# Kernel tuning notes

Measured on AMD Instinct MI355X. Metric: run time of the kernel, lower is better.

The kernel has to match this reference:

```python
import jax, jax.numpy as jnp
from jax import lax
import numpy as np

THRESHOLD = 0.9
KHALF = 5  # conv_kernel_size; full conv width = 2*KHALF + 1 = 11


def _cif_scan(eouts, alpha_norm, elens, ylens, Lp1):
    """Vectorized-over-batch integrate-and-fire scan over time (lax.scan)."""
    B, T, D = eouts.shape
    bidx = jnp.arange(B)
    dt = eouts.dtype

    def step(carry, xs):
        alpha_accum, state, n_tok, fired = carry
        a_t, e_t, t = xs  # a_t: [B], e_t: [B,D], t: scalar int
        alpha_accum = alpha_accum + a_t
        active = (t <= elens - 1) & (n_tok < ylens)
        fire = active & (alpha_accum >= THRESHOLD)
        ak1 = 1.0 - alpha_accum
        ak2 = a_t - ak1
        # attention-weight column for time t
        aw_col = jnp.zeros((B, Lp1), dt)
        w_old = jnp.where(fire, ak1, jnp.where(active, a_t, jnp.zeros((), dt)))
        aw_col = aw_col.at[bidx, n_tok].add(w_old)
        n_new = n_tok + fire.astype(n_tok.dtype)
        aw_col = aw_col.at[bidx, n_new].add(jnp.where(fire, ak2, jnp.zeros((), dt)))
        # fired output row (set once per token slot)
        fire_val = state + ak1[:, None] * e_t
        cur = fired[bidx, n_tok]
        fired = fired.at[bidx, n_tok].set(jnp.where(fire[:, None], fire_val, cur))
        # integrate / reset state
        state = jnp.where(fire[:, None], ak2[:, None] * e_t,
                          jnp.where(active[:, None], state + a_t[:, None] * e_t, state))
        alpha_accum = jnp.where(fire, ak2, alpha_accum)
        return (alpha_accum, state, n_new, fired), aw_col

    init = (jnp.zeros((B,), dt), jnp.zeros((B, D), dt),
            jnp.zeros((B,), jnp.int32), jnp.zeros((B, Lp1, D), dt))
    xs = (jnp.swapaxes(alpha_norm, 0, 1), jnp.swapaxes(eouts, 0, 1),
          jnp.arange(T))
    (_, _, _, fired), aw_cols = lax.scan(step, init, xs)
    aws = jnp.transpose(aw_cols, (1, 2, 0))[:, None]  # [B,1,Lp1,T]
    return fired, aws


def _forward(eouts, conv_w, conv_b, proj_w, proj_b, elens, ylens, L):
    # Conv1d over time, 'same' padding: [B,T,D] -> [B,T,C]
    conv_feat = lax.conv_general_dilated(
        eouts, conv_w, window_strides=(1,), padding=[(KHALF, KHALF)],
        dimension_numbers=('NWC', 'WIO', 'NWC')) + conv_b
    alpha = jax.nn.sigmoid(conv_feat @ proj_w + proj_b)[:, :, 0]  # [B,T]
    alpha_norm = alpha / jnp.sum(alpha, axis=1, keepdims=True) \
        * ylens[:, None].astype(alpha.dtype)
    fired, aws = _cif_scan(eouts, alpha_norm, elens, ylens, L + 1)
    return fired[:, :L], alpha, aws


def setup_inputs():
    key = jax.random.key(0)
    k1, k2, k3, k4, k5 = jax.random.split(key, 5)
    B, T, D, C = 16, 2048, 512, 512
    eouts = jax.random.normal(k1, (B, T, D), jnp.float32)
    elens = jnp.maximum(jax.random.randint(k2, (B,), 0, T), T // 2).astype(jnp.int32)
    ylens = jnp.maximum(jax.random.randint(k3, (B,), 0, 128), 32).astype(jnp.int32)
    conv_w = jax.random.normal(k4, (2 * KHALF + 1, D, C), jnp.float32) * 0.02
    conv_b = jnp.zeros((C,), jnp.float32)
    proj_w = jax.random.normal(k5, (C, 1), jnp.float32) * 0.05
    proj_b = jnp.zeros((1,), jnp.float32)
    return dict(eouts=eouts, conv_w=conv_w, conv_b=conv_b,
                proj_w=proj_w, proj_b=proj_b, elens=elens, ylens=ylens)


def reference(eouts, conv_w, conv_b, proj_w, proj_b, elens, ylens):
    L = int(jnp.max(ylens))  # max_len = ylens.max(), as in the original
    return _forward(eouts, conv_w, conv_b, proj_w, proj_b, elens, ylens, L)
```

## Files before the change

kernel.cpp:

```cpp
#include <hip/hip_runtime.h>
#include <math.h>

#define KHALF 5
#define MAXF 256

__global__ void k_prep(const float* __restrict__ conv_w, const float* __restrict__ conv_b,
                       const float* __restrict__ proj_w, const float* __restrict__ proj_b,
                       float* __restrict__ w_eff, float* __restrict__ b_eff,
                       int KD, int C,
                       float* __restrict__ aws, long long awsN, int WB, int NFILL) {
    if ((int)blockIdx.x >= WB) {
        long long N4 = awsN >> 2;
        long long gid = (long long)(blockIdx.x - WB) * 256 + threadIdx.x;
        float4 z = make_float4(0.f, 0.f, 0.f, 0.f);
        float4* a4 = reinterpret_cast<float4*>(aws);
        long long stride = (long long)NFILL * 256;
        for (long long i = gid; i < N4; i += stride) a4[i] = z;
        int tail = (int)(awsN & 3);
        if (gid < tail) aws[4 * N4 + gid] = 0.f;
        return;
    }
    int gid = blockIdx.x * blockDim.x + threadIdx.x;
    int wave = gid >> 6;
    int lane = gid & 63;
    if (wave > KD) return;
    float s = 0.f;
    if (wave < KD) {
        const float* row = conv_w + (size_t)wave * C;
        for (int c = lane * 4; c < C; c += 256) {
            float4 v = *reinterpret_cast<const float4*>(row + c);
            float4 w = *reinterpret_cast<const float4*>(proj_w + c);
            s += v.x * w.x + v.y * w.y + v.z * w.z + v.w * w.w;
        }
    } else {
        for (int c = lane; c < C; c += 64) s += conv_b[c] * proj_w[c];
    }
#pragma unroll
    for (int off = 32; off > 0; off >>= 1) s += __shfl_down(s, off, 64);
    if (lane == 0) {
        if (wave < KD) w_eff[wave] = s;
        else           b_eff[0] = s + proj_b[0];
    }
}

__global__ __launch_bounds__(256) void k_qdot(const float* __restrict__ eouts,
                                              const float* __restrict__ w_eff,
                                              float* __restrict__ q, int BT) {
    __shared__ float tile[64 * 68];
    __shared__ float wls[11 * 68];
    __shared__ float part[64 * 89];
    const int u0 = blockIdx.x * 64;
    const int rp = threadIdx.x & 31;
    const int s8 = threadIdx.x >> 5;
    float acc0[11], acc1[11];
#pragma unroll
    for (int k = 0; k < 11; ++k) { acc0[k] = 0.f; acc1[k] = 0.f; }
    for (int c = 0; c < 8; ++c) {
        __syncthreads();
#pragma unroll
        for (int it = 0; it < 4; ++it) {
            int idx = it * 256 + threadIdx.x;
            int r = idx >> 4, j4 = idx & 15;
            float4 v = *reinterpret_cast<const float4*>(
                eouts + (size_t)(u0 + r) * 512 + c * 64 + j4 * 4);
            *reinterpret_cast<float4*>(&tile[r * 68 + j4 * 4]) = v;
        }
        if (threadIdx.x < 176) {
            int k = threadIdx.x >> 4, sl = threadIdx.x & 15;
            float4 wv = *reinterpret_cast<const float4*>(
                w_eff + k * 512 + c * 64 + sl * 4);
            *reinterpret_cast<float4*>(&wls[k * 68 + sl * 4]) = wv;
        }
        __syncthreads();
#pragma unroll
        for (int j4 = 0; j4 < 2; ++j4) {
            const int dl = s8 * 8 + j4 * 4;
            float4 a0 = *reinterpret_cast<const float4*>(&tile[rp * 68 + dl]);
            float4 a1 = *reinterpret_cast<const float4*>(&tile[(rp + 32) * 68 + dl]);
#pragma unroll
            for (int k = 0; k < 11; ++k) {
                float4 wv = *reinterpret_cast<const float4*>(&wls[k * 68 + dl]);
                acc0[k] += a0.x * wv.x + a0.y * wv.y + a0.z * wv.z + a0.w * wv.w;
                acc1[k] += a1.x * wv.x + a1.y * wv.y + a1.z * wv.z + a1.w * wv.w;
            }
        }
    }
    __syncthreads();
#pragma unroll
    for (int k = 0; k < 11; ++k) {
        part[rp * 89 + s8 * 11 + k] = acc0[k];
        part[(rp + 32) * 89 + s8 * 11 + k] = acc1[k];
    }
    __syncthreads();
    if (threadIdx.x < 64) {
        int r = threadIdx.x;
        const float* p = &part[r * 89];
        float o[12];
#pragma unroll
        for (int k = 0; k < 11; ++k) {
            float s0 = (p[0 * 11 + k] + p[1 * 11 + k]) + (p[2 * 11 + k] + p[3 * 11 + k]);
            float s1 = (p[4 * 11 + k] + p[5 * 11 + k]) + (p[6 * 11 + k] + p[7 * 11 + k]);
            o[k] = s0 + s1;
        }
        o[11] = 0.f;
        float4* dst = reinterpret_cast<float4*>(q + (size_t)(u0 + r) * 12);
        dst[0] = make_float4(o[0], o[1], o[2], o[3]);
        dst[1] = make_float4(o[4], o[5], o[6], o[7]);
        dst[2] = make_float4(o[8], o[9], o[10], o[11]);
    }
}

__global__ void k_alpha(const float* __restrict__ eouts,
                        const float* __restrict__ w_eff,
                        const float* __restrict__ b_eff,
                        float* __restrict__ alpha,
                        int B, int T, int D) {
    const int W = 2 * KHALF + 1;
    int gid = blockIdx.x * blockDim.x + threadIdx.x;
    int wave = gid >> 6;
    int lane = gid & 63;
    if (wave >= B * T) return;
    int b = wave / T;
    int t = wave - b * T;
    int WD = W * D;
    int t0 = t - KHALF;
    float s = 0.f;
    if (t0 >= 0 && t0 + W <= T) {
        const float* base = eouts + ((size_t)b * T + t0) * D;
        for (int j = lane * 4; j < WD; j += 256) {
            float4 v = *reinterpret_cast<const float4*>(base + j);
            float4 w = *reinterpret_cast<const float4*>(w_eff + j);
            s += v.x * w.x + v.y * w.y + v.z * w.z + v.w * w.w;
        }
    } else {
        const float* base = eouts + (size_t)b * T * D;
        for (int j = lane; j < WD; j += 64) {
            int tt = t0 + j / D;
            if (tt >= 0 && tt < T) {
                int d = j - (j / D) * D;
                s += base[(size_t)tt * D + d] * w_eff[j];
            }
        }
    }
#pragma unroll
    for (int off = 32; off > 0; off >>= 1) s += __shfl_down(s, off, 64);
    if (lane == 0) {
        float logit = s + b_eff[0];
        alpha[(size_t)b * T + t] = 1.f / (1.f + expf(-logit));
    }
}

__global__ void k_chain(const float* __restrict__ alpha_in,
                        const float* __restrict__ qbuf,
                        const float* __restrict__ b_eff,
                        int fused,
                        const int* __restrict__ elens,
                        const int* __restrict__ ylens,
                        float* __restrict__ alpha_out,
                        float* __restrict__ anorm,
                        int* __restrict__ n_fired,
                        int* __restrict__ fire_t,
                        float* __restrict__ fire_a1,
                        float* __restrict__ fire_a2,
                        int T, int Lp1) {
    extern __shared__ float an[];
    float* pf = an + T;
    __shared__ float qs[266 * 12];
    __shared__ float sm[64];
    __shared__ float stot;
    int b = blockIdx.x;
    if (fused) {
        const float* qb = qbuf + (size_t)b * T * 12;
        const int lim = T * 12;
        const int nchunks = T >> 8;
        const float be = b_eff[0];
        for (int c = 0; c < nchunks; ++c) {
            __syncthreads();
            int t0 = c * 256;
            int base = (t0 - 5) * 12;
            for (int i = threadIdx.x; i < 266 * 12; i += 256) {
                int gi = base + i;
                qs[i] = (gi >= 0 && gi < lim) ? qb[gi] : 0.f;
            }
            __syncthreads();
            int t = t0 + threadIdx.x;
            float sacc = be;
#pragma unroll
            for (int k = 0; k < 11; ++k) sacc += qs[(threadIdx.x + k) * 12 + k];
            float al = 1.f / (1.f + expf(-sacc));
            an[t] = al;
            alpha_out[(size_t)b * T + t] = al;
            float s = al;
            int lane = threadIdx.x & 63;
            int w = threadIdx.x >> 6;
#pragma unroll
            for (int off = 32; off > 0; off >>= 1) s += __shfl_down(s, off, 64);
            if (lane == 0) sm[c * 4 + w] = s;
        }
        __syncthreads();
        if (threadIdx.x == 0) {
            float tot = 0.f;
            for (int c = 0; c < nchunks; ++c) {
                float pc = sm[c * 4];
                pc += sm[c * 4 + 1];
                pc += sm[c * 4 + 2];
                pc += sm[c * 4 + 3];
                tot += pc;
            }
            stot = tot;
        }
    } else {
        const float* row = alpha_in + (size_t)b * T;
        for (int i = threadIdx.x; i < T; i += blockDim.x) an[i] = row[i];
        __syncthreads();
        float s = 0.f;
        for (int i = threadIdx.x; i < T; i += blockDim.x) s += an[i];
        int lane0 = threadIdx.x & 63;
        int w0 = threadIdx.x >> 6;
#pragma unroll
        for (int off = 32; off > 0; off >>= 1) s += __shfl_down(s, off, 64);
        if (lane0 == 0) sm[w0] = s;
        __syncthreads();
        if (threadIdx.x == 0) {
            float tot = 0.f;
            int nw = blockDim.x >> 6;
            for (int i = 0; i < nw; ++i) tot += sm[i];
            stot = tot;
        }
    }
    __syncthreads();
    float ssum = stot;
    float yl = (float)ylens[b];
    float* __restrict__ anb = anorm + (size_t)b * T;
    for (int i = threadIdx.x; i < T; i += blockDim.x) {
        float v = an[i] / ssum * yl;
        an[i] = v;
        anb[i] = v;
    }
    __syncthreads();
    {
        int wv = threadIdx.x >> 6, ln = threadIdx.x & 63;
        int nchunks = (T + 63) >> 6;
        for (int c = wv; c < nchunks; c += 4) {
            int t = c * 64 + ln;
            float P = (t < T) ? an[t] : 0.f;
#pragma unroll
            for (int off = 1; off < 64; off <<= 1) {
                float tmp = __shfl_up(P, off, 64);
                if (ln >= off) P += tmp;
            }
            if (t < T) pf[t] = P;
        }
    }
    __syncthreads();
    if (threadIdx.x >= 64) return;
    int lane = threadIdx.x;
    int elen = elens[b];
    if (elen > T) elen = T;
    const int ylen = ylens[b];
    int* __restrict__ ft = fire_t + (size_t)b * Lp1;
    float* __restrict__ fa1 = fire_a1 + (size_t)b * Lp1;
    float* __restrict__ fa2 = fire_a2 + (size_t)b * Lp1;
    float accum = 0.f;
    int n = 0;
    bool done = false;
    for (int t0 = 0; t0 < elen && !done; t0 += 64) {
        int nv = elen - t0;
        if (nv > 64) nv = 64;
        float P = (t0 + lane < T) ? pf[t0 + lane] : 0.f;
        unsigned long long validmask = (nv == 64) ? ~0ull : ((1ull << nv) - 1ull);
        float base = accum;
        int start = 0;
        while (true) {
            bool cond = (base + P >= 0.9f);
            unsigned long long bal = __ballot(cond) & validmask;
            if (start > 0) bal &= (~0ull) << start;
            if (bal == 0) break;
            int u = __builtin_ctzll(bal);
            float Pu = pf[t0 + u];
            float au = an[t0 + u];
            float accum_f = base + Pu;
            float ak1 = 1.f - accum_f;
            float ak2 = au - ak1;
            if (lane == 0) { ft[n] = t0 + u; fa1[n] = ak1; fa2[n] = ak2; }
            ++n;
            if (n >= ylen) { done = true; break; }
            base = ak2 - Pu;
            start = u + 1;
            if (start >= nv) break;
        }
        if (!done) accum = base + pf[t0 + nv - 1];
    }
    if (lane == 0) n_fired[b] = n;
}

__global__ void k_awfired(const float* __restrict__ eouts,
                          const float* __restrict__ anorm,
                          const int* __restrict__ elens,
                          const int* __restrict__ ylens,
                          const int* __restrict__ n_fired,
                          const int* __restrict__ fire_t,
                          const float* __restrict__ fire_a1,
                          const float* __restrict__ fire_a2,
                          float* __restrict__ aws,
                          float* __restrict__ fired,
                          int T, int D, int L, int Lp1,
                          int AB, int tcpb, int nLh) {
    if ((int)blockIdx.x < AB) {
        __shared__ int fts[MAXF];
        __shared__ float a1s[MAXF];
        __shared__ float a2s[MAXF];
        int b = blockIdx.x / tcpb;
        int tc = blockIdx.x % tcpb;
        int nf = n_fired[b];
        for (int i = threadIdx.x; i < nf; i += blockDim.x) {
            fts[i] = fire_t[(size_t)b * Lp1 + i];
            a1s[i] = fire_a1[(size_t)b * Lp1 + i];
            a2s[i] = fire_a2[(size_t)b * Lp1 + i];
        }
        __syncthreads();
        int t = tc * 256 + threadIdx.x;
        if (t >= T) return;
        int elen = elens[b];
        if (elen > T) elen = T;
        int ylen = ylens[b];
        if (t >= elen) return;
        int lo = 0, hi = nf;
        while (lo < hi) {
            int mid = (lo + hi) >> 1;
            if (fts[mid] < t) lo = mid + 1; else hi = mid;
        }
        int rowi = lo;
        bool isfire = (rowi < nf && fts[rowi] == t);
        float* col = aws + (size_t)b * Lp1 * T + t;
        if (isfire) {
            col[(size_t)rowi * T] = a1s[rowi];
            col[(size_t)(rowi + 1) * T] = a2s[rowi];
        } else if (rowi < ylen) {
            col[(size_t)rowi * T] = anorm[(size_t)b * T + t];
        }
    } else {
        int idx = blockIdx.x - AB;
        int b = idx / nLh;
        int j = idx % nLh;
        int half = threadIdx.x >> 7;
        int dl = threadIdx.x & 127;
        int n = 2 * j + half;
        if (n >= L) return;
        int nf = n_fired[b];
        if ((D & 3) == 0) {
            int D4 = D >> 2;
            float4* dst = reinterpret_cast<float4*>(fired + ((size_t)b * L + n) * D);
            if (n >= nf) {
                for (int d4 = dl; d4 < D4; d4 += 128)
                    dst[d4] = make_float4(0.f, 0.f, 0.f, 0.f);
                return;
            }
            int t0 = (n == 0) ? 0 : fire_t[(size_t)b * Lp1 + n - 1];
            int t1 = fire_t[(size_t)b * Lp1 + n];
            float ak1 = fire_a1[(size_t)b * Lp1 + n];
            float ak2p = (n > 0) ? fire_a2[(size_t)b * Lp1 + n - 1] : 0.f;
            const float* an_g = anorm + (size_t)b * T;
            const float4* ebase = reinterpret_cast<const float4*>(
                eouts + ((size_t)b * T + t0) * D);
            for (int d4 = dl; d4 < D4; d4 += 128) {
                const float4* e = ebase + d4;
                float4 accv;
                if (t1 == t0) {
                    float4 v = e[0];
                    accv.x = ak1 * v.x; accv.y = ak1 * v.y;
                    accv.z = ak1 * v.z; accv.w = ak1 * v.w;
                } else {
                    float w0 = (n > 0) ? ak2p : an_g[t0];
                    float4 v = e[0];
                    accv.x = w0 * v.x; accv.y = w0 * v.y;
                    accv.z = w0 * v.z; accv.w = w0 * v.w;
                    float4 a0 = make_float4(0.f, 0.f, 0.f, 0.f);
                    float4 a1 = a0, a2 = a0, a3 = a0;
                    int t = t0 + 1;
                    const float4* ee = e + D4;
                    for (; t + 3 < t1; t += 4, ee += 4 * (size_t)D4) {
                        float wa = an_g[t], wb = an_g[t + 1];
                        float wc = an_g[t + 2], wd = an_g[t + 3];
                        float4 va = ee[0], vb = ee[D4], vc = ee[2 * (size_t)D4], vd = ee[3 * (size_t)D4];
                        a0.x += wa * va.x; a0.y += wa * va.y; a0.z += wa * va.z; a0.w += wa * va.w;
                        a1.x += wb * vb.x; a1.y += wb * vb.y; a1.z += wb * vb.z; a1.w += wb * vb.w;
                        a2.x += wc * vc.x; a2.y += wc * vc.y; a2.z += wc * vc.z; a2.w += wc * vc.w;
                        a3.x += wd * vd.x; a3.y += wd * vd.y; a3.z += wd * vd.z; a3.w += wd * vd.w;
                    }
                    for (; t < t1; ++t, ee += D4) {
                        float wa = an_g[t];
                        float4 va = ee[0];
                        a0.x += wa * va.x; a0.y += wa * va.y; a0.z += wa * va.z; a0.w += wa * va.w;
                    }
                    accv.x += ((a0.x + a1.x) + (a2.x + a3.x));
                    accv.y += ((a0.y + a1.y) + (a2.y + a3.y));
                    accv.z += ((a0.z + a1.z) + (a2.z + a3.z));
                    accv.w += ((a0.w + a1.w) + (a2.w + a3.w));
                    float4 vl = ee[0];
                    accv.x += ak1 * vl.x; accv.y += ak1 * vl.y;
                    accv.z += ak1 * vl.z; accv.w += ak1 * vl.w;
                }
                dst[d4] = accv;
            }
        } else {
            float* dst = fired + ((size_t)b * L + n) * D;
            if (n >= nf) {
                for (int d = dl; d < D; d += 128) dst[d] = 0.f;
                return;
            }
            int t0 = (n == 0) ? 0 : fire_t[(size_t)b * Lp1 + n - 1];
            int t1 = fire_t[(size_t)b * Lp1 + n];
            float ak1 = fire_a1[(size_t)b * Lp1 + n];
            float ak2p = (n > 0) ? fire_a2[(size_t)b * Lp1 + n - 1] : 0.f;
            const float* an_g = anorm + (size_t)b * T;
            for (int d = dl; d < D; d += 128) {
                const float* e = eouts + ((size_t)b * T + t0) * D + d;
                float accv;
                if (t1 == t0) {
                    accv = ak1 * e[0];
                } else {
                    float w0 = (n > 0) ? ak2p : an_g[t0];
                    accv = w0 * e[0];
                    float a0 = 0.f, a1 = 0.f, a2 = 0.f, a3 = 0.f;
                    int t = t0 + 1;
                    const float* ee = e + D;
                    for (; t + 3 < t1; t += 4, ee += 4 * (size_t)D) {
                        a0 += an_g[t]     * ee[0];
                        a1 += an_g[t + 1] * ee[D];
                        a2 += an_g[t + 2] * ee[2 * (size_t)D];
                        a3 += an_g[t + 3] * ee[3 * (size_t)D];
                    }
                    for (; t < t1; ++t, ee += D) a0 += an_g[t] * ee[0];
                    accv += ((a0 + a1) + (a2 + a3));
                    accv += ak1 * ee[0];
                }
                dst[d] = accv;
            }
        }
    }
}

extern "C" void kernel_launch(void* const* d_in, const int* in_sizes, int n_in,
                              void* d_out, int out_size, void* d_ws, size_t ws_size,
                              hipStream_t stream) {
    const float* eouts  = (const float*)d_in[0];
    const float* conv_w = (const float*)d_in[1];
    const float* conv_b = (const float*)d_in[2];
    const float* proj_w = (const float*)d_in[3];
    const float* proj_b = (const float*)d_in[4];
    const int*   elens  = (const int*)d_in[5];
    const int*   ylens  = (const int*)d_in[6];

    const int B = in_sizes[5];
    const int C = in_sizes[2];
    const int W = 2 * KHALF + 1;
    const int D = in_sizes[1] / (W * C);
    const int T = in_sizes[0] / (B * D);
    const int L = (out_size - 2 * B * T) / (B * (D + T));
    const int Lp1 = L + 1;
    const int BT = B * T;

    float* out   = (float*)d_out;
    float* fired = out;
    float* alpha = out + (size_t)B * L * D;
    float* aws   = alpha + (size_t)B * T;

    char*  ws        = (char*)d_ws;
    float* w_eff     = (float*)ws;
    float* b_eff     = (float*)(ws + (size_t)W * D * 4);
    int*   n_fired   = (int*)(b_eff + 16);
    int*   fire_t    = n_fired + B + 16;
    float* fire_a1   = (float*)(fire_t + (size_t)B * Lp1 + 16);
    float* fire_a2   = fire_a1 + (size_t)B * Lp1 + 16;
    float* anorm     = fire_a2 + (size_t)B * Lp1 + 16;
    float* qbuf      = anorm + (size_t)B * T + 16;
    size_t ws_need   = (size_t)((char*)(qbuf + (size_t)BT * 12 + 16) - ws);

    const int KD = W * D;
    {
        long long wthreads = (long long)(KD + 1) * 64;
        int WB = (int)((wthreads + 255) / 256);
        int NFILL = 2048;
        long long awsN = (long long)B * Lp1 * T;
        k_prep<<<WB + NFILL, 256, 0, stream>>>(conv_w, conv_b, proj_w, proj_b,
                                               w_eff, b_eff, KD, C,
                                               aws, awsN, WB, NFILL);
    }

    const bool fast = (ws_size >= ws_need) && (D == 512) && (C == 512) &&
                      (BT % 64 == 0) && (T % 256 == 0) && (T <= 16384) &&
                      (Lp1 <= MAXF);
    if (fast) {
        k_qdot<<<BT / 64, 256, 0, stream>>>(eouts, w_eff, qbuf, BT);
        k_chain<<<B, 256, 2 * T * sizeof(float), stream>>>(
            nullptr, qbuf, b_eff, 1,
            elens, ylens, alpha, anorm,
            n_fired, fire_t, fire_a1, fire_a2, T, Lp1);
    } else {
        long long threads = (long long)BT * 64;
        int blocks = (int)((threads + 255) / 256);
        k_alpha<<<blocks, 256, 0, stream>>>(eouts, w_eff, b_eff, alpha, B, T, D);
        k_chain<<<B, 256, 2 * T * sizeof(float), stream>>>(
            alpha, nullptr, nullptr, 0,
            elens, ylens, alpha, anorm,
            n_fired, fire_t, fire_a1, fire_a2, T, Lp1);
    }

    {
        int tcpb = (T + 255) / 256;
        int AB = B * tcpb;
        int nLh = (L + 1) / 2;
        if (nLh < 1) nLh = 1;
        int FB = B * nLh;
        k_awfired<<<AB + FB, 256, 0, stream>>>(eouts, anorm,
                                               elens, ylens, n_fired,
                                               fire_t, fire_a1, fire_a2,
                                               aws, fired, T, D, L, Lp1,
                                               AB, tcpb, nLh);
    }
}
```

Measured before the change: 189.5 us.

## Split alpha sigmoid into parallel kernel and use readlane in fire scan

Moves the sigmoid/alpha computation and per-chunk partial sums out of the per-batch serial chain kernel into a separate kernel launched over B*T/256 blocks, so this work is no longer done by only B blocks looping over chunks. The chain kernel then reloads alpha with vector loads and sums the partials. The fire scan also reads P and alpha from registers via readlane instead of LDS. It adds a kernel launch and a global round-trip for alpha.

```diff
diff --git a/kernel.cpp b/kernel.cpp
--- a/kernel.cpp
+++ b/kernel.cpp
@@ -3,6 +3,10 @@
 
 #define KHALF 5
 #define MAXF 256
+
+__device__ inline float readlane_f(float v, int lane) {
+    return __int_as_float(__builtin_amdgcn_readlane(__float_as_int(v), lane));
+}
 
 __global__ void k_prep(const float* __restrict__ conv_w, const float* __restrict__ conv_b,
                        const float* __restrict__ proj_w, const float* __restrict__ proj_b,
@@ -107,6 +111,44 @@
         dst[0] = make_float4(o[0], o[1], o[2], o[3]);
         dst[1] = make_float4(o[4], o[5], o[6], o[7]);
         dst[2] = make_float4(o[8], o[9], o[10], o[11]);
+    }
+}
+
+__global__ __launch_bounds__(256) void k_sigpart(const float* __restrict__ q,
+                                                 const float* __restrict__ b_eff,
+                                                 float* __restrict__ alpha,
+                                                 float* __restrict__ partials,
+                                                 int T, int tcb) {
+    __shared__ float qs[266 * 12];
+    __shared__ float psm[4];
+    int bx = blockIdx.x;
+    int b = bx / tcb, tc = bx % tcb;
+    int t0 = tc * 256;
+    const float* qb = q + (size_t)b * T * 12;
+    const int base = (t0 - 5) * 12;
+    const int lim = T * 12;
+    for (int i = threadIdx.x; i < 266 * 12; i += 256) {
+        int gi = base + i;
+        qs[i] = (gi >= 0 && gi < lim) ? qb[gi] : 0.f;
+    }
+    __syncthreads();
+    int t = t0 + threadIdx.x;
+    float sacc = b_eff[0];
+#pragma unroll
+    for (int k = 0; k < 11; ++k) sacc += qs[(threadIdx.x + k) * 12 + k];
+    float al = 1.f / (1.f + expf(-sacc));
+    alpha[(size_t)b * T + t] = al;
+    float s = al;
+    int lane = threadIdx.x & 63;
+    int w = threadIdx.x >> 6;
+#pragma unroll
+    for (int off = 32; off > 0; off >>= 1) s += __shfl_down(s, off, 64);
+    if (lane == 0) psm[w] = s;
+    __syncthreads();
+    if (threadIdx.x == 0) {
+        float tot = 0.f;
+        for (int i = 0; i < 4; ++i) tot += psm[i];
+        partials[bx] = tot;
     }
 }
 
@@ -151,12 +193,10 @@
 }
 
 __global__ void k_chain(const float* __restrict__ alpha_in,
-                        const float* __restrict__ qbuf,
-                        const float* __restrict__ b_eff,
-                        int fused,
+                        int use_part,
+                        const float* __restrict__ partials, int npart,
                         const int* __restrict__ elens,
                         const int* __restrict__ ylens,
-                        float* __restrict__ alpha_out,
                         float* __restrict__ anorm,
                         int* __restrict__ n_fired,
                         int* __restrict__ fire_t,
@@ -165,54 +205,29 @@
                         int T, int Lp1) {
     extern __shared__ float an[];
     float* pf = an + T;
-    __shared__ float qs[266 * 12];
-    __shared__ float sm[64];
+    __shared__ float sm[16];
     __shared__ float stot;
     int b = blockIdx.x;
-    if (fused) {
-        const float* qb = qbuf + (size_t)b * T * 12;
-        const int lim = T * 12;
-        const int nchunks = T >> 8;
-        const float be = b_eff[0];
-        for (int c = 0; c < nchunks; ++c) {
-            __syncthreads();
-            int t0 = c * 256;
-            int base = (t0 - 5) * 12;
-            for (int i = threadIdx.x; i < 266 * 12; i += 256) {
-                int gi = base + i;
-                qs[i] = (gi >= 0 && gi < lim) ? qb[gi] : 0.f;
-            }
-            __syncthreads();
-            int t = t0 + threadIdx.x;
-            float sacc = be;
-#pragma unroll
-            for (int k = 0; k < 11; ++k) sacc += qs[(threadIdx.x + k) * 12 + k];
-            float al = 1.f / (1.f + expf(-sacc));
-            an[t] = al;
-            alpha_out[(size_t)b * T + t] = al;
-            float s = al;
-            int lane = threadIdx.x & 63;
-            int w = threadIdx.x >> 6;
-#pragma unroll
-            for (int off = 32; off > 0; off >>= 1) s += __shfl_down(s, off, 64);
-            if (lane == 0) sm[c * 4 + w] = s;
-        }
+    const float* row = alpha_in + (size_t)b * T;
+    if ((T & 1023) == 0) {
+        const float4* r4 = reinterpret_cast<const float4*>(row);
+        float4* a4 = reinterpret_cast<float4*>(an);
+        for (int i = threadIdx.x; i < (T >> 2); i += blockDim.x) a4[i] = r4[i];
+    } else {
+        for (int i = threadIdx.x; i < T; i += blockDim.x) an[i] = row[i];
+    }
+    __syncthreads();
+    if (use_part) {
+        if (threadIdx.x < npart && threadIdx.x < 16)
+            sm[threadIdx.x] = partials[b * npart + threadIdx.x];
         __syncthreads();
         if (threadIdx.x == 0) {
             float tot = 0.f;
-            for (int c = 0; c < nchunks; ++c) {
-                float pc = sm[c * 4];
-                pc += sm[c * 4 + 1];
-                pc += sm[c * 4 + 2];
-                pc += sm[c * 4 + 3];
-                tot += pc;
-            }
+            if (npart <= 16) { for (int i = 0; i < npart; ++i) tot += sm[i]; }
+            else { for (int i = 0; i < npart; ++i) tot += partials[b * npart + i]; }
             stot = tot;
         }
     } else {
-        const float* row = alpha_in + (size_t)b * T;
-        for (int i = threadIdx.x; i < T; i += blockDim.x) an[i] = row[i];
-        __syncthreads();
         float s = 0.f;
         for (int i = threadIdx.x; i < T; i += blockDim.x) s += an[i];
         int lane0 = threadIdx.x & 63;
@@ -267,7 +282,9 @@
     for (int t0 = 0; t0 < elen && !done; t0 += 64) {
         int nv = elen - t0;
         if (nv > 64) nv = 64;
-        float P = (t0 + lane < T) ? pf[t0 + lane] : 0.f;
+        bool inb = (t0 + lane < T);
+        float P = inb ? pf[t0 + lane] : 0.f;
+        float av = inb ? an[t0 + lane] : 0.f;
         unsigned long long validmask = (nv == 64) ? ~0ull : ((1ull << nv) - 1ull);
         float base = accum;
         int start = 0;
@@ -277,8 +294,8 @@
             if (start > 0) bal &= (~0ull) << start;
             if (bal == 0) break;
             int u = __builtin_ctzll(bal);
-            float Pu = pf[t0 + u];
-            float au = an[t0 + u];
+            float Pu = readlane_f(P, u);
+            float au = readlane_f(av, u);
             float accum_f = base + Pu;
             float ak1 = 1.f - accum_f;
             float ak2 = au - ak1;
@@ -289,7 +306,7 @@
             start = u + 1;
             if (start >= nv) break;
         }
-        if (!done) accum = base + pf[t0 + nv - 1];
+        if (!done) accum = base + readlane_f(P, nv - 1);
     }
     if (lane == 0) n_fired[b] = n;
 }
@@ -460,6 +477,7 @@
     const int L = (out_size - 2 * B * T) / (B * (D + T));
     const int Lp1 = L + 1;
     const int BT = B * T;
+    const int tcb = (T + 255) / 256;
 
     float* out   = (float*)d_out;
     float* fired = out;
@@ -475,7 +493,8 @@
     float* fire_a2   = fire_a1 + (size_t)B * Lp1 + 16;
     float* anorm     = fire_a2 + (size_t)B * Lp1 + 16;
     float* qbuf      = anorm + (size_t)B * T + 16;
-    size_t ws_need   = (size_t)((char*)(qbuf + (size_t)BT * 12 + 16) - ws);
+    float* partials  = qbuf + (size_t)BT * 12 + 16;
+    size_t ws_need   = (size_t)((char*)(partials + (size_t)B * tcb + 16) - ws);
 
     const int KD = W * D;
     {
@@ -493,19 +512,17 @@
                       (Lp1 <= MAXF);
     if (fast) {
         k_qdot<<<BT / 64, 256, 0, stream>>>(eouts, w_eff, qbuf, BT);
-        k_chain<<<B, 256, 2 * T * sizeof(float), stream>>>(
-            nullptr, qbuf, b_eff, 1,
-            elens, ylens, alpha, anorm,
-            n_fired, fire_t, fire_a1, fire_a2, T, Lp1);
+        k_sigpart<<<B * tcb, 256, 0, stream>>>(qbuf, b_eff, alpha, partials, T, tcb);
     } else {
         long long threads = (long long)BT * 64;
         int blocks = (int)((threads + 255) / 256);
         k_alpha<<<blocks, 256, 0, stream>>>(eouts, w_eff, b_eff, alpha, B, T, D);
-        k_chain<<<B, 256, 2 * T * sizeof(float), stream>>>(
-            alpha, nullptr, nullptr, 0,
-            elens, ylens, alpha, anorm,
-            n_fired, fire_t, fire_a1, fire_a2, T, Lp1);
-    }
+    }
+
+    k_chain<<<B, 256, 2 * T * sizeof(float), stream>>>(
+        alpha, fast ? 1 : 0, partials, tcb,
+        elens, ylens, anorm,
+        n_fired, fire_t, fire_a1, fire_a2, T, Lp1);
 
     {
         int tcpb = (T + 255) / 256;
```

New measurement: 159.9 us, median of 2. 15.6% less time.
